# Optimization experiments

Hardware: AMD Instinct MI355X
Metric: run time of the kernel (lower is better)

Reference implementation:

```python
import jax, jax.numpy as jnp
import numpy as np

DIM = 1024
MEM_DIM = 1024
BANK = 8192
B, S = 4, 4096
LN_EPS = 1e-5


def setup_inputs() -> dict:
    key = jax.random.key(0)
    ks = jax.random.split(key, 8)
    std_q = 1.0 / np.sqrt(DIM)
    std_m = 1.0 / np.sqrt(MEM_DIM)
    std_f = 1.0 / np.sqrt(DIM + MEM_DIM)
    return {
        "x": jax.random.normal(ks[0], (B, S, DIM), jnp.float32),
        "knowledge_bank": 0.02 * jax.random.normal(ks[1], (BANK, MEM_DIM), jnp.float32),
        "wq": std_q * jax.random.normal(ks[2], (MEM_DIM, DIM), jnp.float32),
        "bq": jnp.zeros((MEM_DIM,), jnp.float32),
        "wk": std_m * jax.random.normal(ks[3], (MEM_DIM, MEM_DIM), jnp.float32),
        "bk": jnp.zeros((MEM_DIM,), jnp.float32),
        "wv": std_m * jax.random.normal(ks[4], (DIM, MEM_DIM), jnp.float32),
        "bv": jnp.zeros((DIM,), jnp.float32),
        "wf": std_f * jax.random.normal(ks[5], (DIM, DIM + MEM_DIM), jnp.float32),
        "bf": jnp.zeros((DIM,), jnp.float32),
        "gamma": jnp.ones((DIM,), jnp.float32),
        "beta": jnp.zeros((DIM,), jnp.float32),
    }


def reference(x, knowledge_bank, wq, bq, wk, bk, wv, bv, wf, bf, gamma, beta):
    # queries: [B,S,MEM_DIM]; keys/values over the fixed bank: [BANK, *]
    queries = jnp.einsum("bsd,md->bsm", x, wq) + bq
    keys = jnp.einsum("nd,md->nm", knowledge_bank, wk) + bk
    values = jnp.einsum("nd,md->nm", knowledge_bank, wv) + bv
    scores = jnp.einsum("bsm,nm->bsn", queries, keys) / jnp.sqrt(
        jnp.asarray(MEM_DIM, x.dtype)
    )
    attn = jax.nn.softmax(scores, axis=-1)  # [B,S,BANK]
    retrieved = jnp.einsum("bsn,nd->bsd", attn, values)  # [B,S,DIM]
    combined = jnp.concatenate([x, retrieved], axis=-1)  # [B,S,2*DIM]
    out = jnp.einsum("bsc,dc->bsd", combined, wf) + bf
    h = out + x
    # LayerNorm over last dim, eps = 1e-5 (torch default)
    mu = jnp.mean(h, axis=-1, keepdims=True)
    var = jnp.mean(jnp.square(h - mu), axis=-1, keepdims=True)
    return (h - mu) * jax.lax.rsqrt(var + LN_EPS) * gamma + beta
```

## Files before the change

### kernel.cpp

```cpp
#include <hip/hip_runtime.h>


typedef __bf16 bf16;
typedef __bf16 bf16x4 __attribute__((ext_vector_type(4)));
typedef __bf16 bf16x8 __attribute__((ext_vector_type(8)));
typedef float f32x4 __attribute__((ext_vector_type(4)));

static __device__ __forceinline__ f32x4 mfma16(bf16x8 a, bf16x8 b, f32x4 c) {
  return __builtin_amdgcn_mfma_f32_16x16x32_bf16(a, b, c, 0, 0, 0);
}

#define GLDS16(gp, lp) __builtin_amdgcn_global_load_lds( \
    (const __attribute__((address_space(1))) void*)(gp), \
    (__attribute__((address_space(3))) void*)(lp), 16, 0, 0)

template<int EPI, int CONCAT>
__global__ __launch_bounds__(256, 3) void gemm_bb(
    const bf16* __restrict__ A, const bf16* __restrict__ A2,
    const bf16* __restrict__ W, const float* __restrict__ bias,
    const float* __restrict__ resid, float* __restrict__ L,
    void* __restrict__ Cout, int N, int K)
{
  __shared__ bf16 As[128 * 64];
  __shared__ bf16 Bs[128 * 64];
  const int tid = threadIdx.x, lane = tid & 63, wid = tid >> 6;
  const int wm = (wid >> 1) * 64, wn = (wid & 1) * 64;
  const int quad = lane >> 4, l16 = lane & 15;
  const long bm = (long)blockIdx.y * 128, bn = (long)blockIdx.x * 128;

  int prow[4], pcg[4];
#pragma unroll
  for (int i = 0; i < 4; ++i) {
    int p = ((wid * 4 + i) << 6) + lane;
    prow[i] = p >> 3;
    pcg[i] = (p & 7) ^ (prow[i] & 7);
  }

  f32x4 acc[4][4] = {};

  for (int k0 = 0; k0 < K; k0 += 64) {
    const bf16* Asrc = (CONCAT && k0 >= 1024) ? A2 : A;
    const int kA = (CONCAT && k0 >= 1024) ? k0 - 1024 : k0;
    const int lda = CONCAT ? 1024 : K;
    __syncthreads();
#pragma unroll
    for (int i = 0; i < 4; ++i) {
      const bf16* ga = Asrc + (size_t)(bm + prow[i]) * lda + kA + pcg[i] * 8;
      GLDS16(ga, (char*)As + ((wid * 4 + i) << 10));
    }
#pragma unroll
    for (int i = 0; i < 4; ++i) {
      const bf16* gb = W + (size_t)(bn + prow[i]) * K + k0 + pcg[i] * 8;
      GLDS16(gb, (char*)Bs + ((wid * 4 + i) << 10));
    }
    __syncthreads();
#pragma unroll
    for (int kk = 0; kk < 2; ++kk) {
      bf16x8 af[4], bfv[4];
#pragma unroll
      for (int mt = 0; mt < 4; ++mt) {
        const int r = wm + mt * 16 + l16;
        af[mt] = *(const bf16x8*)((const char*)As + (r << 7)
                                  + ((((kk << 2) + quad) ^ (r & 7)) << 4));
      }
#pragma unroll
      for (int nt = 0; nt < 4; ++nt) {
        const int r = wn + nt * 16 + l16;
        bfv[nt] = *(const bf16x8*)((const char*)Bs + (r << 7)
                                   + ((((kk << 2) + quad) ^ (r & 7)) << 4));
      }
#pragma unroll
      for (int mt = 0; mt < 4; ++mt)
#pragma unroll
        for (int nt = 0; nt < 4; ++nt)
          acc[mt][nt] = mfma16(af[mt], bfv[nt], acc[mt][nt]);
    }
  }

#pragma unroll
  for (int mt = 0; mt < 4; ++mt) {
    const long row0 = bm + wm + mt * 16 + quad * 4;
    if (EPI == 2) {
      float rsum[4] = {0.f, 0.f, 0.f, 0.f};
#pragma unroll
      for (int nt = 0; nt < 4; ++nt) {
        const long col = bn + wn + nt * 16 + l16;
#pragma unroll
        for (int r = 0; r < 4; ++r) {
          float p = __expf(acc[mt][nt][r] * 0.03125f);
          rsum[r] += p;
          ((bf16*)Cout)[(size_t)(row0 + r) * N + col] = (bf16)p;
        }
      }
#pragma unroll
      for (int s = 1; s < 16; s <<= 1)
#pragma unroll
        for (int r = 0; r < 4; ++r) rsum[r] += __shfl_xor(rsum[r], s, 64);
      if (l16 == 0) {
#pragma unroll
        for (int r = 0; r < 4; ++r) atomicAdd(&L[row0 + r], rsum[r]);
      }
    } else {
#pragma unroll
      for (int nt = 0; nt < 4; ++nt) {
        const long col = bn + wn + nt * 16 + l16;
        const float bc = (EPI == 1) ? 0.f : bias[col];
#pragma unroll
        for (int r = 0; r < 4; ++r) {
          float v = acc[mt][nt][r] + ((EPI == 1) ? bias[row0 + r] : bc);
          if (EPI == 3) {
            v += resid[(size_t)(row0 + r) * 1024 + col];
            ((float*)Cout)[(size_t)(row0 + r) * N + col] = v;
          } else {
            ((bf16*)Cout)[(size_t)(row0 + r) * N + col] = (bf16)v;
          }
        }
      }
    }
  }
}

__global__ __launch_bounds__(512, 2) void pv_gemm(
    const bf16* __restrict__ P, const bf16* __restrict__ Vt,
    const float* __restrict__ L, bf16* __restrict__ Rb)
{
  __shared__ bf16 As[128 * 128];
  __shared__ bf16 Bs[128 * 128];
  const int tid = threadIdx.x, lane = tid & 63, wid = tid >> 6;
  const int wm = (wid & 3) * 32, wn = (wid >> 2) * 64;
  const int quad = lane >> 4, l16 = lane & 15;
  const long bm = (long)blockIdx.y * 128, bn = (long)blockIdx.x * 128;

  int prow[4], pcg[4];
#pragma unroll
  for (int i = 0; i < 4; ++i) {
    int p = ((wid * 4 + i) << 6) + lane;
    prow[i] = p >> 4;
    pcg[i] = (p & 15) ^ (prow[i] & 15);
  }

  f32x4 acc[2][4] = {};

  for (int k0 = 0; k0 < 8192; k0 += 128) {
    __syncthreads();
#pragma unroll
    for (int i = 0; i < 4; ++i)
      GLDS16(P + (size_t)(bm + prow[i]) * 8192 + k0 + pcg[i] * 8,
             (char*)As + ((wid * 4 + i) << 10));
#pragma unroll
    for (int i = 0; i < 4; ++i)
      GLDS16(Vt + (size_t)(bn + prow[i]) * 8192 + k0 + pcg[i] * 8,
             (char*)Bs + ((wid * 4 + i) << 10));
    __syncthreads();
#pragma unroll
    for (int kk = 0; kk < 4; ++kk) {
      bf16x8 af[2], bfv[4];
#pragma unroll
      for (int mt = 0; mt < 2; ++mt) {
        const int r = wm + mt * 16 + l16;
        af[mt] = *(const bf16x8*)((const char*)As + (r << 8)
                                  + ((((kk << 2) + quad) ^ (r & 15)) << 4));
      }
#pragma unroll
      for (int nt = 0; nt < 4; ++nt) {
        const int r = wn + nt * 16 + l16;
        bfv[nt] = *(const bf16x8*)((const char*)Bs + (r << 8)
                                   + ((((kk << 2) + quad) ^ (r & 15)) << 4));
      }
#pragma unroll
      for (int mt = 0; mt < 2; ++mt)
#pragma unroll
        for (int nt = 0; nt < 4; ++nt)
          acc[mt][nt] = mfma16(af[mt], bfv[nt], acc[mt][nt]);
    }
  }

#pragma unroll
  for (int mt = 0; mt < 2; ++mt) {
    const long row0 = bm + wm + mt * 16 + quad * 4;
    float linv[4];
#pragma unroll
    for (int r = 0; r < 4; ++r) linv[r] = 1.f / L[row0 + r];
#pragma unroll
    for (int nt = 0; nt < 4; ++nt) {
      const long col = bn + wn + nt * 16 + l16;
#pragma unroll
      for (int r = 0; r < 4; ++r)
        Rb[(size_t)(row0 + r) * 1024 + col] = (bf16)(acc[mt][nt][r] * linv[r]);
    }
  }
}

template<int BIAS_ROW, int OUT_F32_RES, int CONCAT>
__global__ __launch_bounds__(256, 3) void gemm_nt(
    const float* __restrict__ A, const bf16* __restrict__ A2,
    const float* __restrict__ W, const float* __restrict__ bias,
    const float* __restrict__ resid, void* __restrict__ Cout,
    int M, int N, int K)
{
  __shared__ bf16 As[128][72];
  __shared__ bf16 Bs[128][72];
  const int tid  = threadIdx.x;
  const int lane = tid & 63;
  const int wid  = tid >> 6;
  const int wm   = (wid >> 1) * 64, wn = (wid & 1) * 64;
  const int quad = lane >> 4, l16 = lane & 15;
  const long bm = (long)blockIdx.y * 128, bn = (long)blockIdx.x * 128;
  const int r0 = tid >> 2, cq = (tid & 3) * 16;
  const int lda = CONCAT ? 1024 : K;

  f32x4 acc[4][4] = {};

  for (int k0 = 0; k0 < K; k0 += 64) {
    const bool useb = CONCAT && (k0 >= 1024);
    const int kA = useb ? (k0 - 1024) : k0;
    f32x4 va[2][4], vb[2][4];
    bf16x8 ra[2][2];
    if (useb) {
#pragma unroll
      for (int g = 0; g < 2; ++g) {
        const bf16* p = A2 + (size_t)(bm + r0 + 64 * g) * 1024 + kA + cq;
        ra[g][0] = *(const bf16x8*)p;
        ra[g][1] = *(const bf16x8*)(p + 8);
      }
    } else {
#pragma unroll
      for (int g = 0; g < 2; ++g) {
        const f32x4* p = (const f32x4*)(A + (size_t)(bm + r0 + 64 * g) * lda + kA + cq);
#pragma unroll
        for (int j = 0; j < 4; ++j) va[g][j] = p[j];
      }
    }
#pragma unroll
    for (int g = 0; g < 2; ++g) {
      const f32x4* p = (const f32x4*)(W + (size_t)(bn + r0 + 64 * g) * K + k0 + cq);
#pragma unroll
      for (int j = 0; j < 4; ++j) vb[g][j] = p[j];
    }
    __syncthreads();
#pragma unroll
    for (int g = 0; g < 2; ++g) {
      bf16* dA = &As[r0 + 64 * g][cq];
      if (useb) {
        *(bf16x8*)dA = ra[g][0]; *(bf16x8*)(dA + 8) = ra[g][1];
      } else {
        bf16x8 t0, t1;
#pragma unroll
        for (int j = 0; j < 4; ++j) {
          t0[j] = (bf16)va[g][0][j]; t0[4 + j] = (bf16)va[g][1][j];
          t1[j] = (bf16)va[g][2][j]; t1[4 + j] = (bf16)va[g][3][j];
        }
        *(bf16x8*)dA = t0; *(bf16x8*)(dA + 8) = t1;
      }
      bf16* dB = &Bs[r0 + 64 * g][cq];
      bf16x8 u0, u1;
#pragma unroll
      for (int j = 0; j < 4; ++j) {
        u0[j] = (bf16)vb[g][0][j]; u0[4 + j] = (bf16)vb[g][1][j];
        u1[j] = (bf16)vb[g][2][j]; u1[4 + j] = (bf16)vb[g][3][j];
      }
      *(bf16x8*)dB = u0; *(bf16x8*)(dB + 8) = u1;
    }
    __syncthreads();
#pragma unroll
    for (int kk = 0; kk < 2; ++kk) {
      bf16x8 af[4], bfv[4];
#pragma unroll
      for (int mt = 0; mt < 4; ++mt)
        af[mt] = *(const bf16x8*)&As[wm + mt * 16 + l16][kk * 32 + quad * 8];
#pragma unroll
      for (int nt = 0; nt < 4; ++nt)
        bfv[nt] = *(const bf16x8*)&Bs[wn + nt * 16 + l16][kk * 32 + quad * 8];
#pragma unroll
      for (int mt = 0; mt < 4; ++mt)
#pragma unroll
        for (int nt = 0; nt < 4; ++nt)
          acc[mt][nt] = mfma16(af[mt], bfv[nt], acc[mt][nt]);
    }
  }
#pragma unroll
  for (int mt = 0; mt < 4; ++mt) {
    const long row0 = bm + wm + mt * 16 + quad * 4;
#pragma unroll
    for (int nt = 0; nt < 4; ++nt) {
      const long col = bn + wn + nt * 16 + l16;
      const float bc = BIAS_ROW ? 0.f : bias[col];
#pragma unroll
      for (int r = 0; r < 4; ++r) {
        float v = acc[mt][nt][r] + (BIAS_ROW ? bias[row0 + r] : bc);
        if (OUT_F32_RES) {
          v += resid[(size_t)(row0 + r) * 1024 + col];
          ((float*)Cout)[(size_t)(row0 + r) * N + col] = v;
        } else {
          ((bf16*)Cout)[(size_t)(row0 + r) * N + col] = (bf16)v;
        }
      }
    }
  }
}

__global__ __launch_bounds__(256) void cvt6(
    const float* __restrict__ x, const float* __restrict__ bank,
    const float* __restrict__ wq, const float* __restrict__ wk,
    const float* __restrict__ wv, const float* __restrict__ wf,
    bf16* __restrict__ xb, bf16* __restrict__ bankb,
    bf16* __restrict__ wqb, bf16* __restrict__ wkb,
    bf16* __restrict__ wvb, bf16* __restrict__ wfb)
{
  long i4 = (long)blockIdx.x * 256 + threadIdx.x;
  const float* src; bf16* dst; long off;
  if      (i4 < 4194304) { src = x;    dst = xb;    off = i4; }
  else if (i4 < 6291456) { src = bank; dst = bankb; off = i4 - 4194304; }
  else if (i4 < 6553600) { src = wq;   dst = wqb;   off = i4 - 6291456; }
  else if (i4 < 6815744) { src = wk;   dst = wkb;   off = i4 - 6553600; }
  else if (i4 < 7077888) { src = wv;   dst = wvb;   off = i4 - 6815744; }
  else if (i4 < 7602176) { src = wf;   dst = wfb;   off = i4 - 7077888; }
  else return;
  f32x4 v = ((const f32x4*)src)[off];
  bf16x4 o;
#pragma unroll
  for (int j = 0; j < 4; ++j) o[j] = (bf16)v[j];
  ((bf16x4*)dst)[off] = o;
}

__global__ __launch_bounds__(256) void zerof(float* __restrict__ p) {
  p[(size_t)blockIdx.x * 256 + threadIdx.x] = 0.f;
}

__global__ __launch_bounds__(256) void ln_kernel(
    float* __restrict__ h, const float* __restrict__ g, const float* __restrict__ b)
{
  const int tid = threadIdx.x;
  const size_t row = blockIdx.x;
  f32x4 v = *(f32x4*)&h[row * 1024 + tid * 4];
  float s1 = v[0] + v[1] + v[2] + v[3];
  float s2 = v[0]*v[0] + v[1]*v[1] + v[2]*v[2] + v[3]*v[3];
#pragma unroll
  for (int d = 1; d < 64; d <<= 1) { s1 += __shfl_xor(s1, d, 64); s2 += __shfl_xor(s2, d, 64); }
  __shared__ float a1[4], a2[4];
  const int wid = tid >> 6;
  if ((tid & 63) == 0) { a1[wid] = s1; a2[wid] = s2; }
  __syncthreads();
  s1 = a1[0] + a1[1] + a1[2] + a1[3];
  s2 = a2[0] + a2[1] + a2[2] + a2[3];
  const float mu = s1 * (1.f / 1024.f);
  const float rs = rsqrtf(s2 * (1.f / 1024.f) - mu * mu + 1e-5f);
  f32x4 gv = *(const f32x4*)&g[tid * 4];
  f32x4 bv = *(const f32x4*)&b[tid * 4];
#pragma unroll
  for (int j = 0; j < 4; ++j) v[j] = (v[j] - mu) * rs * gv[j] + bv[j];
  *(f32x4*)&h[row * 1024 + tid * 4] = v;
}

extern "C" void kernel_launch(void* const* d_in, const int* in_sizes, int n_in,
                              void* d_out, int out_size, void* d_ws, size_t ws_size,
                              hipStream_t stream)
{
  const float* x     = (const float*)d_in[0];
  const float* kbank = (const float*)d_in[1];
  const float* wq    = (const float*)d_in[2];
  const float* bq    = (const float*)d_in[3];
  const float* wk    = (const float*)d_in[4];
  const float* bk    = (const float*)d_in[5];
  const float* wv    = (const float*)d_in[6];
  const float* bv    = (const float*)d_in[7];
  const float* wf    = (const float*)d_in[8];
  const float* bf_   = (const float*)d_in[9];
  const float* gamma = (const float*)d_in[10];
  const float* beta  = (const float*)d_in[11];

  char* ws = (char*)d_ws;
  const size_t MB = 1024 * 1024;
  bf16*  Qb    = (bf16*)ws;
  bf16*  Rb    = Qb;
  bf16*  Kb    = (bf16*)(ws + 32 * MB);
  bf16*  Vt    = (bf16*)(ws + 48 * MB);
  float* L     = (float*)(ws + 64 * MB);
  bf16*  xb    = (bf16*)(ws + 65 * MB);
  bf16*  bankb = (bf16*)(ws + 97 * MB);
  bf16*  wfb   = (bf16*)(ws + 113 * MB);
  bf16*  wqb   = (bf16*)(ws + 117 * MB);
  bf16*  wkb   = (bf16*)(ws + 119 * MB);
  bf16*  wvb   = (bf16*)(ws + 121 * MB);
  bf16*  P     = (bf16*)d_out;
  float* out   = (float*)d_out;
  const bool big = ws_size >= 123 * MB;

  if (big) {
    cvt6<<<dim3(29696), dim3(256), 0, stream>>>(
        x, kbank, wq, wk, wv, wf, xb, bankb, wqb, wkb, wvb, wfb);
    gemm_bb<0,0><<<dim3(8, 128), dim3(256), 0, stream>>>(
        xb, nullptr, wqb, bq, nullptr, nullptr, (void*)Qb, 1024, 1024);
    gemm_bb<0,0><<<dim3(8, 64), dim3(256), 0, stream>>>(
        bankb, nullptr, wkb, bk, nullptr, nullptr, (void*)Kb, 1024, 1024);
    gemm_bb<1,0><<<dim3(64, 8), dim3(256), 0, stream>>>(
        wvb, nullptr, bankb, bv, nullptr, nullptr, (void*)Vt, 8192, 1024);
  } else {
    gemm_nt<0,0,0><<<dim3(8, 128), dim3(256), 0, stream>>>(
        x, nullptr, wq, bq, nullptr, (void*)Qb, 16384, 1024, 1024);
    gemm_nt<0,0,0><<<dim3(8, 64), dim3(256), 0, stream>>>(
        kbank, nullptr, wk, bk, nullptr, (void*)Kb, 8192, 1024, 1024);
    gemm_nt<1,0,0><<<dim3(64, 8), dim3(256), 0, stream>>>(
        wv, nullptr, kbank, bv, nullptr, (void*)Vt, 1024, 8192, 1024);
  }

  zerof<<<dim3(64), dim3(256), 0, stream>>>(L);
  for (int c = 0; c < 4; ++c) {
    gemm_bb<2,0><<<dim3(64, 32), dim3(256), 0, stream>>>(
        Qb + (size_t)c * 4096 * 1024, nullptr, Kb, nullptr, nullptr,
        L + c * 4096, (void*)P, 8192, 1024);
    pv_gemm<<<dim3(8, 32), dim3(512), 0, stream>>>(
        P, Vt, L + c * 4096, Rb + (size_t)c * 4096 * 1024);
  }

  if (big) {
    gemm_bb<3,1><<<dim3(8, 128), dim3(256), 0, stream>>>(
        xb, Rb, wfb, bf_, x, nullptr, (void*)out, 1024, 2048);
  } else {
    gemm_nt<0,1,1><<<dim3(8, 128), dim3(256), 0, stream>>>(
        x, Rb, wf, bf_, x, (void*)out, 16384, 1024, 2048);
  }
  ln_kernel<<<dim3(16384), dim3(256), 0, stream>>>(out, gamma, beta);
}
```

Baseline: 1.167 ms.

## Chunk attention over bank keys with bf16 running accumulator and final normalize

The fast path now splits attention into eight chunks over the bank's keys instead of four chunks over the queries. Each chunk computes exp-scores for all queries against 1024 keys, then runs a generic bf16 GEMM that multiplies them by the matching slice of the transposed values. That GEMM uses a new leading-dimension argument and adds its result into a bf16 running accumulator. A new pv_norm kernel divides the accumulator by the softmax denominators before the final fused projection. The aim is to reuse the tuned gemm_bb tile in place of the separate pv_gemm kernel. The cost is an extra read and write of the full accumulator for every chunk, and a precision risk from summing partial results in bf16.

Result: no change. 1.174 ms (+0.6%).

```diff
diff --git a/kernel.cpp b/kernel.cpp
--- a/kernel.cpp
+++ b/kernel.cpp
@@ -19,7 +19,7 @@
     const bf16* __restrict__ A, const bf16* __restrict__ A2,
     const bf16* __restrict__ W, const float* __restrict__ bias,
     const float* __restrict__ resid, float* __restrict__ L,
-    void* __restrict__ Cout, int N, int K)
+    void* __restrict__ Cout, int N, int K, int ldw)
 {
   __shared__ bf16 As[128 * 64];
   __shared__ bf16 Bs[128 * 64];
@@ -50,7 +50,7 @@
     }
 #pragma unroll
     for (int i = 0; i < 4; ++i) {
-      const bf16* gb = W + (size_t)(bn + prow[i]) * K + k0 + pcg[i] * 8;
+      const bf16* gb = W + (size_t)(bn + prow[i]) * ldw + k0 + pcg[i] * 8;
       GLDS16(gb, (char*)Bs + ((wid * 4 + i) << 10));
     }
     __syncthreads();
@@ -99,6 +99,18 @@
       if (l16 == 0) {
 #pragma unroll
         for (int r = 0; r < 4; ++r) atomicAdd(&L[row0 + r], rsum[r]);
+      }
+    } else if (EPI == 4 || EPI == 5) {
+#pragma unroll
+      for (int nt = 0; nt < 4; ++nt) {
+        const long col = bn + wn + nt * 16 + l16;
+#pragma unroll
+        for (int r = 0; r < 4; ++r) {
+          float v = acc[mt][nt][r];
+          if (EPI == 5)
+            v += (float)((const bf16*)resid)[(size_t)(row0 + r) * N + col];
+          ((bf16*)Cout)[(size_t)(row0 + r) * N + col] = (bf16)v;
+        }
       }
     } else {
 #pragma unroll
@@ -325,6 +337,20 @@
 
 __global__ __launch_bounds__(256) void zerof(float* __restrict__ p) {
   p[(size_t)blockIdx.x * 256 + threadIdx.x] = 0.f;
+}
+
+__global__ __launch_bounds__(256) void pv_norm(
+    const bf16* __restrict__ Racc, const float* __restrict__ L,
+    bf16* __restrict__ Rout)
+{
+  const size_t row = blockIdx.x;
+  const float linv = 1.f / L[row];
+  const int t = threadIdx.x;
+  bf16x4 v = ((const bf16x4*)(Racc + row * 1024))[t];
+  bf16x4 o;
+#pragma unroll
+  for (int j = 0; j < 4; ++j) o[j] = (bf16)((float)v[j] * linv);
+  ((bf16x4*)(Rout + row * 1024))[t] = o;
 }
 
 __global__ __launch_bounds__(256) void ln_kernel(
@@ -375,6 +401,7 @@
   bf16*  Rb    = Qb;
   bf16*  Kb    = (bf16*)(ws + 32 * MB);
   bf16*  Vt    = (bf16*)(ws + 48 * MB);
+  bf16*  Rfin  = (bf16*)(ws + 32 * MB);
   float* L     = (float*)(ws + 64 * MB);
   bf16*  xb    = (bf16*)(ws + 65 * MB);
   bf16*  bankb = (bf16*)(ws + 97 * MB);
@@ -383,6 +410,7 @@
   bf16*  wkb   = (bf16*)(ws + 119 * MB);
   bf16*  wvb   = (bf16*)(ws + 121 * MB);
   bf16*  P     = (bf16*)d_out;
+  bf16*  Racc  = (bf16*)((char*)d_out + 32 * MB);
   float* out   = (float*)d_out;
   const bool big = ws_size >= 123 * MB;
 
@@ -390,11 +418,30 @@
     cvt6<<<dim3(29696), dim3(256), 0, stream>>>(
         x, kbank, wq, wk, wv, wf, xb, bankb, wqb, wkb, wvb, wfb);
     gemm_bb<0,0><<<dim3(8, 128), dim3(256), 0, stream>>>(
-        xb, nullptr, wqb, bq, nullptr, nullptr, (void*)Qb, 1024, 1024);
+        xb, nullptr, wqb, bq, nullptr, nullptr, (void*)Qb, 1024, 1024, 1024);
     gemm_bb<0,0><<<dim3(8, 64), dim3(256), 0, stream>>>(
-        bankb, nullptr, wkb, bk, nullptr, nullptr, (void*)Kb, 1024, 1024);
+        bankb, nullptr, wkb, bk, nullptr, nullptr, (void*)Kb, 1024, 1024, 1024);
     gemm_bb<1,0><<<dim3(64, 8), dim3(256), 0, stream>>>(
-        wvb, nullptr, bankb, bv, nullptr, nullptr, (void*)Vt, 8192, 1024);
+        wvb, nullptr, bankb, bv, nullptr, nullptr, (void*)Vt, 8192, 1024, 1024);
+    zerof<<<dim3(64), dim3(256), 0, stream>>>(L);
+
+    for (int c = 0; c < 8; ++c) {
+      gemm_bb<2,0><<<dim3(8, 128), dim3(256), 0, stream>>>(
+          Qb, nullptr, Kb + (size_t)c * 1024 * 1024, nullptr, nullptr,
+          L, (void*)P, 1024, 1024, 1024);
+      if (c == 0)
+        gemm_bb<4,0><<<dim3(8, 128), dim3(256), 0, stream>>>(
+            P, nullptr, Vt + (size_t)c * 1024, nullptr, nullptr, nullptr,
+            (void*)Racc, 1024, 1024, 8192);
+      else
+        gemm_bb<5,0><<<dim3(8, 128), dim3(256), 0, stream>>>(
+            P, nullptr, Vt + (size_t)c * 1024, nullptr, (const float*)Racc,
+            nullptr, (void*)Racc, 1024, 1024, 8192);
+    }
+    pv_norm<<<dim3(16384), dim3(256), 0, stream>>>(Racc, L, Rfin);
+
+    gemm_bb<3,1><<<dim3(8, 128), dim3(256), 0, stream>>>(
+        xb, Rfin, wfb, bf_, x, nullptr, (void*)out, 1024, 2048, 2048);
   } else {
     gemm_nt<0,0,0><<<dim3(8, 128), dim3(256), 0, stream>>>(
         x, nullptr, wq, bq, nullptr, (void*)Qb, 16384, 1024, 1024);
@@ -402,21 +449,14 @@
         kbank, nullptr, wk, bk, nullptr, (void*)Kb, 8192, 1024, 1024);
     gemm_nt<1,0,0><<<dim3(64, 8), dim3(256), 0, stream>>>(
         wv, nullptr, kbank, bv, nullptr, (void*)Vt, 1024, 8192, 1024);
-  }
-
-  zerof<<<dim3(64), dim3(256), 0, stream>>>(L);
-  for (int c = 0; c < 4; ++c) {
-    gemm_bb<2,0><<<dim3(64, 32), dim3(256), 0, stream>>>(
-        Qb + (size_t)c * 4096 * 1024, nullptr, Kb, nullptr, nullptr,
-        L + c * 4096, (void*)P, 8192, 1024);
-    pv_gemm<<<dim3(8, 32), dim3(512), 0, stream>>>(
-        P, Vt, L + c * 4096, Rb + (size_t)c * 4096 * 1024);
-  }
-
-  if (big) {
-    gemm_bb<3,1><<<dim3(8, 128), dim3(256), 0, stream>>>(
-        xb, Rb, wfb, bf_, x, nullptr, (void*)out, 1024, 2048);
-  } else {
+    zerof<<<dim3(64), dim3(256), 0, stream>>>(L);
+    for (int c = 0; c < 4; ++c) {
+      gemm_bb<2,0><<<dim3(64, 32), dim3(256), 0, stream>>>(
+          Qb + (size_t)c * 4096 * 1024, nullptr, Kb, nullptr, nullptr,
+          L + c * 4096, (void*)P, 8192, 1024, 1024);
+      pv_gemm<<<dim3(8, 32), dim3(512), 0, stream>>>(
+          P, Vt, L + c * 4096, Rb + (size_t)c * 4096 * 1024);
+    }
     gemm_nt<0,1,1><<<dim3(8, 128), dim3(256), 0, stream>>>(
         x, Rb, wf, bf_, x, (void*)out, 16384, 1024, 2048);
   }
```

## Double-buffer PV GEMM LDS tiles and add XCD-aware block swizzle

Applied to the files above, without the earlier changes.

pv_gemm now stages the next 128-wide K tile into a second LDS buffer while computing on the current one, which removes one barrier per iteration. It also raises wave priority around the MFMA section. Both GEMM kernels remap block indices so that neighbouring tiles land on the same XCD, aiming for better L2 reuse. In exchange, pv_gemm's LDS use doubles to 128KB, which may cut occupancy, and a pass-through ldw parameter is added with a redundant if/else branch.

Result: faster. 1.087 ms (-6.9%).

```diff
diff --git a/kernel.cpp b/kernel.cpp
--- a/kernel.cpp
+++ b/kernel.cpp
@@ -13,20 +13,29 @@
 #define GLDS16(gp, lp) __builtin_amdgcn_global_load_lds( \
     (const __attribute__((address_space(1))) void*)(gp), \
     (__attribute__((address_space(3))) void*)(lp), 16, 0, 0)
+
+static __device__ __forceinline__ void xcd_swizzle(long& bm, long& bn) {
+  const int nwg = (int)(gridDim.x * gridDim.y);
+  int flat = (int)(blockIdx.y * gridDim.x + blockIdx.x);
+  flat = (flat & 7) * (nwg >> 3) + (flat >> 3);
+  bm = (long)(flat / (int)gridDim.x) * 128;
+  bn = (long)(flat % (int)gridDim.x) * 128;
+}
 
 template<int EPI, int CONCAT>
 __global__ __launch_bounds__(256, 3) void gemm_bb(
     const bf16* __restrict__ A, const bf16* __restrict__ A2,
     const bf16* __restrict__ W, const float* __restrict__ bias,
     const float* __restrict__ resid, float* __restrict__ L,
-    void* __restrict__ Cout, int N, int K)
+    void* __restrict__ Cout, int N, int K, int ldw)
 {
   __shared__ bf16 As[128 * 64];
   __shared__ bf16 Bs[128 * 64];
   const int tid = threadIdx.x, lane = tid & 63, wid = tid >> 6;
   const int wm = (wid >> 1) * 64, wn = (wid & 1) * 64;
   const int quad = lane >> 4, l16 = lane & 15;
-  const long bm = (long)blockIdx.y * 128, bn = (long)blockIdx.x * 128;
+  long bm, bn;
+  xcd_swizzle(bm, bn);
 
   int prow[4], pcg[4];
 #pragma unroll
@@ -50,7 +59,7 @@
     }
 #pragma unroll
     for (int i = 0; i < 4; ++i) {
-      const bf16* gb = W + (size_t)(bn + prow[i]) * K + k0 + pcg[i] * 8;
+      const bf16* gb = W + (size_t)(bn + prow[i]) * ldw + k0 + pcg[i] * 8;
       GLDS16(gb, (char*)Bs + ((wid * 4 + i) << 10));
     }
     __syncthreads();
@@ -124,12 +133,13 @@
     const bf16* __restrict__ P, const bf16* __restrict__ Vt,
     const float* __restrict__ L, bf16* __restrict__ Rb)
 {
-  __shared__ bf16 As[128 * 128];
-  __shared__ bf16 Bs[128 * 128];
+  __shared__ bf16 As[2][128 * 128];
+  __shared__ bf16 Bs[2][128 * 128];
   const int tid = threadIdx.x, lane = tid & 63, wid = tid >> 6;
   const int wm = (wid & 3) * 32, wn = (wid >> 2) * 64;
   const int quad = lane >> 4, l16 = lane & 15;
-  const long bm = (long)blockIdx.y * 128, bn = (long)blockIdx.x * 128;
+  long bm, bn;
+  xcd_swizzle(bm, bn);
 
   int prow[4], pcg[4];
 #pragma unroll
@@ -141,30 +151,32 @@
 
   f32x4 acc[2][4] = {};
 
-  for (int k0 = 0; k0 < 8192; k0 += 128) {
-    __syncthreads();
+  auto stage = [&](int buf, int k0) {
 #pragma unroll
     for (int i = 0; i < 4; ++i)
       GLDS16(P + (size_t)(bm + prow[i]) * 8192 + k0 + pcg[i] * 8,
-             (char*)As + ((wid * 4 + i) << 10));
+             (char*)As[buf] + ((wid * 4 + i) << 10));
 #pragma unroll
     for (int i = 0; i < 4; ++i)
       GLDS16(Vt + (size_t)(bn + prow[i]) * 8192 + k0 + pcg[i] * 8,
-             (char*)Bs + ((wid * 4 + i) << 10));
-    __syncthreads();
+             (char*)Bs[buf] + ((wid * 4 + i) << 10));
+  };
+
+  auto compute = [&](int buf) {
+    __builtin_amdgcn_s_setprio(1);
 #pragma unroll
     for (int kk = 0; kk < 4; ++kk) {
       bf16x8 af[2], bfv[4];
 #pragma unroll
       for (int mt = 0; mt < 2; ++mt) {
         const int r = wm + mt * 16 + l16;
-        af[mt] = *(const bf16x8*)((const char*)As + (r << 8)
+        af[mt] = *(const bf16x8*)((const char*)As[buf] + (r << 8)
                                   + ((((kk << 2) + quad) ^ (r & 15)) << 4));
       }
 #pragma unroll
       for (int nt = 0; nt < 4; ++nt) {
         const int r = wn + nt * 16 + l16;
-        bfv[nt] = *(const bf16x8*)((const char*)Bs + (r << 8)
+        bfv[nt] = *(const bf16x8*)((const char*)Bs[buf] + (r << 8)
                                    + ((((kk << 2) + quad) ^ (r & 15)) << 4));
       }
 #pragma unroll
@@ -173,7 +185,19 @@
         for (int nt = 0; nt < 4; ++nt)
           acc[mt][nt] = mfma16(af[mt], bfv[nt], acc[mt][nt]);
     }
-  }
+    __builtin_amdgcn_s_setprio(0);
+  };
+
+  stage(0, 0);
+  __syncthreads();
+  int cur = 0;
+  for (int t = 0; t < 63; ++t) {
+    stage(cur ^ 1, (t + 1) * 128);
+    compute(cur);
+    __syncthreads();
+    cur ^= 1;
+  }
+  compute(cur);
 
 #pragma unroll
   for (int mt = 0; mt < 2; ++mt) {
@@ -390,11 +414,11 @@
     cvt6<<<dim3(29696), dim3(256), 0, stream>>>(
         x, kbank, wq, wk, wv, wf, xb, bankb, wqb, wkb, wvb, wfb);
     gemm_bb<0,0><<<dim3(8, 128), dim3(256), 0, stream>>>(
-        xb, nullptr, wqb, bq, nullptr, nullptr, (void*)Qb, 1024, 1024);
+        xb, nullptr, wqb, bq, nullptr, nullptr, (void*)Qb, 1024, 1024, 1024);
     gemm_bb<0,0><<<dim3(8, 64), dim3(256), 0, stream>>>(
-        bankb, nullptr, wkb, bk, nullptr, nullptr, (void*)Kb, 1024, 1024);
+        bankb, nullptr, wkb, bk, nullptr, nullptr, (void*)Kb, 1024, 1024, 1024);
     gemm_bb<1,0><<<dim3(64, 8), dim3(256), 0, stream>>>(
-        wvb, nullptr, bankb, bv, nullptr, nullptr, (void*)Vt, 8192, 1024);
+        wvb, nullptr, bankb, bv, nullptr, nullptr, (void*)Vt, 8192, 1024, 1024);
   } else {
     gemm_nt<0,0,0><<<dim3(8, 128), dim3(256), 0, stream>>>(
         x, nullptr, wq, bq, nullptr, (void*)Qb, 16384, 1024, 1024);
@@ -406,16 +430,21 @@
 
   zerof<<<dim3(64), dim3(256), 0, stream>>>(L);
   for (int c = 0; c < 4; ++c) {
-    gemm_bb<2,0><<<dim3(64, 32), dim3(256), 0, stream>>>(
-        Qb + (size_t)c * 4096 * 1024, nullptr, Kb, nullptr, nullptr,
-        L + c * 4096, (void*)P, 8192, 1024);
+    if (big)
+      gemm_bb<2,0><<<dim3(64, 32), dim3(256), 0, stream>>>(
+          Qb + (size_t)c * 4096 * 1024, nullptr, Kb, nullptr, nullptr,
+          L + c * 4096, (void*)P, 8192, 1024, 1024);
+    else
+      gemm_bb<2,0><<<dim3(64, 32), dim3(256), 0, stream>>>(
+          Qb + (size_t)c * 4096 * 1024, nullptr, Kb, nullptr, nullptr,
+          L + c * 4096, (void*)P, 8192, 1024, 1024);
     pv_gemm<<<dim3(8, 32), dim3(512), 0, stream>>>(
         P, Vt, L + c * 4096, Rb + (size_t)c * 4096 * 1024);
   }
 
   if (big) {
     gemm_bb<3,1><<<dim3(8, 128), dim3(256), 0, stream>>>(
-        xb, Rb, wfb, bf_, x, nullptr, (void*)out, 1024, 2048);
+        xb, Rb, wfb, bf_, x, nullptr, (void*)out, 1024, 2048, 2048);
   } else {
     gemm_nt<0,1,1><<<dim3(8, 128), dim3(256), 0, stream>>>(
         x, Rb, wf, bf_, x, (void*)out, 16384, 1024, 2048);
```
